# Kernel tuning notes

Measured on AMD Instinct MI355X. Metric: run time of the kernel, lower is better.

## Reference

```python
import jax, jax.numpy as jnp
import numpy as np

NUM_GROUPS = 4   # temporal frames == deformable groups
K = 3            # deformable / fusion kernel size
PAD = 1
MAX_DISP = 7
STRIDE2 = 2


def _conv2d(x, w):
    # 3x3, stride 1, pad 1, no bias, NCHW/OIHW
    return jax.lax.conv_general_dilated(
        x, w, window_strides=(1, 1), padding=((PAD, PAD), (PAD, PAD)),
        dimension_numbers=("NCHW", "OIHW", "NCHW"))


def _correlation(x1, x2):
    """FlowNet/PWC correlation: kernel_size=1, max_displacement=7, stride1=1, stride2=2.
    Output: [B, 49, H, W], mean over channels of shifted dot products."""
    B, C, H, W = x1.shape
    r = MAX_DISP // STRIDE2          # 3 -> 7x7 displacement grid
    m = r * STRIDE2                  # 6 = max shift magnitude
    x2p = jnp.pad(x2, ((0, 0), (0, 0), (m, m), (m, m)))
    outs = []
    for di in range(-r, r + 1):
        for dj in range(-r, r + 1):
            dy, dx = di * STRIDE2, dj * STRIDE2
            sh = x2p[:, :, m + dy:m + dy + H, m + dx:m + dx + W]
            outs.append(jnp.mean(x1 * sh, axis=1))
    return jnp.stack(outs, axis=1)   # [B, 49, H, W]


def _deform_conv(x, offset, weight):
    """Deformable conv v1 (ConvOffset2d): 3x3, stride 1, pad 1, NUM_GROUPS deformable groups.
    offset: [B, G*2*K*K, H, W] laid out as (g, k, {dy,dx})."""
    B, C, H, W = x.shape
    G, K2 = NUM_GROUPS, K * K
    Cg = C // G
    off = offset.reshape(B, G, K2, 2, H, W)
    rel = (jnp.arange(K) - PAD).astype(x.dtype)
    rel_y = jnp.repeat(rel, K).reshape(1, 1, K2, 1, 1)   # kh-major, matches weight flatten
    rel_x = jnp.tile(rel, K).reshape(1, 1, K2, 1, 1)
    iy = jnp.arange(H, dtype=x.dtype).reshape(1, 1, 1, H, 1)
    ix = jnp.arange(W, dtype=x.dtype).reshape(1, 1, 1, 1, W)
    py = iy + rel_y + off[:, :, :, 0]   # [B,G,K2,H,W] sample rows
    px = ix + rel_x + off[:, :, :, 1]   # sample cols
    xg = x.reshape(B, G, Cg, H, W).transpose(0, 1, 3, 4, 2)  # [B,G,H,W,Cg]
    y0 = jnp.floor(py); x0 = jnp.floor(px)
    fy = py - y0; fx = px - x0
    y0 = y0.astype(jnp.int32); x0 = x0.astype(jnp.int32)
    bi = jnp.arange(B).reshape(B, 1, 1, 1, 1)
    gi = jnp.arange(G).reshape(1, G, 1, 1, 1)
    acc = jnp.zeros((B, G, K2, H, W, Cg), x.dtype)
    for dy in (0, 1):
        for dx in (0, 1):
            yy = y0 + dy; xx = x0 + dx
            wgt = (fy if dy else 1.0 - fy) * (fx if dx else 1.0 - fx)
            valid = ((yy >= 0) & (yy < H) & (xx >= 0) & (xx < W)).astype(x.dtype)
            v = xg[bi, gi, jnp.clip(yy, 0, H - 1), jnp.clip(xx, 0, W - 1)]
            acc = acc + v * (wgt * valid)[..., None]
    wr = weight.reshape(weight.shape[0], G, Cg, K2)  # [O,G,Cg,K2]
    return jnp.einsum('bgkhwc,ogck->bohw', acc, wr)


def setup_inputs() -> dict:
    key = jax.random.key(0)
    k0, k1, k2, k3 = jax.random.split(key, 4)
    B, C, H, W = 4, 256, 64, 64
    G = NUM_GROUPS
    inputs = jax.random.normal(k0, (B * G, C, H, W), jnp.float32)
    w_offset = jax.random.normal(k1, (G * 2 * K * K, C + MAX_DISP ** 2, K, K), jnp.float32) * 0.02
    w_def = jax.random.normal(k2, (C, C, K, K), jnp.float32) * 0.02
    w_fusion = jax.random.normal(k3, (C, C * G, K, K), jnp.float32) * 0.02
    return {"inputs": inputs, "w_offset": w_offset, "w_def": w_def,
            "w_fusion": w_fusion, "d1": 0, "d2": 0}


def reference(inputs, w_offset, w_def, w_fusion, d1, d2):
    # d1, d2 are unused by the original forward.
    G = NUM_GROUPS
    y = inputs[G - 1::G]
    _y = jax.lax.stop_gradient(y)
    feats = []
    for ii in range(G - 1):           # n_iter = 1
        x = inputs[ii::G]
        _x = jax.lax.stop_gradient(x)
        corr = _correlation(_x, _y)                       # [B,49,H,W]
        off = _conv2d(jnp.concatenate([x, corr], axis=1), w_offset)
        x = _deform_conv(x, off, w_def)
        feats.append(x)
    return _conv2d(jnp.concatenate(feats + [y], axis=1), w_fusion)
```

## Files before the change

### kernel.cpp

```cpp
#include <hip/hip_runtime.h>

#define HH 64
#define WW 64
#define HW 4096
#define CC 256
#define BB 4
#define GG 4
#define NPAIR 3

typedef __attribute__((ext_vector_type(8))) short short8;
typedef __attribute__((ext_vector_type(4))) float f32x4;
typedef unsigned short ushort_t;

__device__ inline ushort_t f2bf(float x) {
    unsigned int u = __float_as_uint(x);
    unsigned int r = (u + 0x7fffu + ((u >> 16) & 1u)) >> 16;
    return (ushort_t)r;
}
__device__ inline float bflo(unsigned u) { return __uint_as_float(u << 16); }
__device__ inline float bfhi(unsigned u) { return __uint_as_float(u & 0xffff0000u); }

__global__ void prep_all(const float* __restrict__ wd, const float* __restrict__ wo,
                         const float* __restrict__ wf, ushort_t* __restrict__ wdefMF,
                         ushort_t* __restrict__ woffMF, ushort_t* __restrict__ wfusMF) {
    int idx = blockIdx.x * 256 + threadIdx.x;
    if (idx < 589824) {
        int k = idx >> 16;
        int rem = idx & 65535;
        int o = rem >> 8;
        int c = rem & 255;
        wdefMF[idx] = f2bf(wd[((size_t)(o * 256 + c)) * 9 + k]);
        return;
    }
    idx -= 589824;
    if (idx < 230400) {
        int k = idx / (80 * 320);
        int rem = idx % (80 * 320);
        int o = rem / 320;
        int ci = rem % 320;
        woffMF[idx] = (o < 72 && ci < 305) ? f2bf(wo[((size_t)o * 305 + ci) * 9 + k])
                                           : (ushort_t)0;
        return;
    }
    idx -= 230400;
    if (idx < 2359296) {
        int k = idx / (256 * 1024);
        int rem = idx % (256 * 1024);
        int o = rem / 1024;
        int ci = rem % 1024;
        wfusMF[idx] = f2bf(wf[((size_t)o * 1024 + ci) * 9 + k]);
    }
}

__global__ void __launch_bounds__(256) xt_build(const float* __restrict__ in,
                                                ushort_t* __restrict__ XT) {
    __shared__ ushort_t tileT[64][72];
    int hw0 = blockIdx.x * 64;
    int ct = blockIdx.y;
    int z = blockIdx.z;
    int pair = z >> 2, b = z & 3;
    int t = threadIdx.x;
    int cil = t >> 2, q = t & 3;
    const float* sp = in + ((size_t)(b * 4 + pair) * 256 + ct * 64 + cil) * HW + hw0 + q * 16;
#pragma unroll
    for (int i = 0; i < 16; ++i) tileT[q * 16 + i][cil] = f2bf(sp[i]);
    __syncthreads();
    int hwl = t >> 2;
    const uint4* tp = reinterpret_cast<const uint4*>(&tileT[hwl][q * 16]);
    uint4* op = reinterpret_cast<uint4*>(
        &XT[((size_t)z * HW + hw0 + hwl) * 320 + ct * 64 + q * 16]);
    op[0] = tp[0];
    op[1] = tp[1];
}

__global__ void __launch_bounds__(256, 8) corr_partial(const float* __restrict__ in,
                                                       float* __restrict__ P) {
    __shared__ float x1l[8][64];
    __shared__ float x2l[8][7][76];
    int h = blockIdx.x, z = blockIdx.y, cg = blockIdx.z;
    int pair = z >> 2, b = z & 3;
    const float* x1 = in + (size_t)(b * GG + pair) * CC * HW + h * WW;
    const float* x2 = in + (size_t)(b * GG + 3) * CC * HW;
    int tid = threadIdx.x;
    int w = tid & 63;
    int dg = tid >> 6;

    float acc[2][7];
#pragma unroll
    for (int i = 0; i < 2; ++i)
#pragma unroll
        for (int j = 0; j < 7; ++j) acc[i][j] = 0.f;

    for (int c0 = cg * 64; c0 < cg * 64 + 64; c0 += 8) {
        __syncthreads();
#pragma unroll
        for (int idx = tid; idx < 512; idx += 256) {
            int cc = idx >> 6, ww = idx & 63;
            x1l[cc][ww] = x1[(size_t)(c0 + cc) * HW + ww];
        }
        for (int idx = tid; idx < 8 * 7 * 76; idx += 256) {
            int cc = idx / 532;
            int rem = idx - cc * 532;
            int r = rem / 76;
            int cl = rem - r * 76;
            int row = h + 2 * (r - 3);
            int col = cl - 6;
            float v = 0.f;
            if (row >= 0 && row < HH && col >= 0 && col < WW)
                v = x2[(size_t)(c0 + cc) * HW + row * WW + col];
            x2l[cc][r][cl] = v;
        }
        __syncthreads();
#pragma unroll
        for (int cc = 0; cc < 8; ++cc) {
            float x1v = x1l[cc][w];
#pragma unroll
            for (int i = 0; i < 2; ++i) {
                int di = dg * 2 + i;
                if (di < 7) {
#pragma unroll
                    for (int dj = 0; dj < 7; ++dj)
                        acc[i][dj] += x1v * x2l[cc][di][w + 2 * dj];
                }
            }
        }
    }
    float* pp = P + ((size_t)(cg * 12 + z) * 49) * HW + h * WW + w;
#pragma unroll
    for (int i = 0; i < 2; ++i) {
        int di = dg * 2 + i;
        if (di < 7) {
#pragma unroll
            for (int dj = 0; dj < 7; ++dj)
                pp[(size_t)(di * 7 + dj) * HW] = acc[i][dj];
        }
    }
}

__global__ void __launch_bounds__(256) corr_reduce(const float* __restrict__ P,
                                                   ushort_t* __restrict__ XT) {
    int h = blockIdx.x, z = blockIdx.y;
    int tid = threadIdx.x;
    int w = tid & 63;
    int dg = tid >> 6;
    const size_t cgs = (size_t)12 * 49 * HW;
    ushort_t* xrow = XT + ((size_t)z * HW + h * WW + w) * 320;
#pragma unroll
    for (int i = 0; i < 2; ++i) {
        int di = dg * 2 + i;
        if (di < 7) {
#pragma unroll
            for (int dj = 0; dj < 7; ++dj) {
                int d = di * 7 + dj;
                const float* pp = P + ((size_t)z * 49 + d) * HW + h * WW + w;
                float s = pp[0] + pp[cgs] + pp[2 * cgs] + pp[3 * cgs];
                xrow[256 + d] = f2bf(s * (1.f / 256.f));
            }
        }
    }
    if (dg == 3) {
#pragma unroll
        for (int p = 0; p < 15; ++p) xrow[305 + p] = 0;
    }
}

__global__ void __launch_bounds__(256, 2) offconv_mfma(const ushort_t* __restrict__ XT,
                                                       const ushort_t* __restrict__ wmf,
                                                       float* __restrict__ off) {
    __shared__ ushort_t a_lds[9][80][40];
    __shared__ ushort_t b_hal[264][40];
    int lin = (blockIdx.x & 7) * 48 + (blockIdx.x >> 3);
    int z = lin >> 5;
    int n0t = lin & 31;
    int h0 = n0t * 2;
    int t = threadIdx.x;
    int wid = t >> 6;
    int lane = t & 63;
    int l15 = lane & 15;
    int kq = lane >> 4;
    const ushort_t* xtb = XT + (size_t)z * HW * 320;

    f32x4 acc[5][2];
#pragma unroll
    for (int m = 0; m < 5; ++m)
#pragma unroll
        for (int n = 0; n < 2; ++n) acc[m][n] = (f32x4){0.f, 0.f, 0.f, 0.f};

#pragma unroll 1
    for (int cs = 0; cs < 10; ++cs) {
        int ci0 = cs * 32;
        __syncthreads();
        for (int idx = t; idx < 264; idx += 256) {
            int r = idx / 66, c = idx - r * 66;
            int hP = h0 + r - 1, wP = c - 1;
            uint4* dst = reinterpret_cast<uint4*>(&b_hal[idx][0]);
            if (hP >= 0 && hP < HH && wP >= 0 && wP < WW) {
                const uint4* src = reinterpret_cast<const uint4*>(
                    xtb + (size_t)(hP * WW + wP) * 320 + ci0);
                dst[0] = src[0];
                dst[1] = src[1];
                dst[2] = src[2];
                dst[3] = src[3];
            } else {
                uint4 zz = make_uint4(0, 0, 0, 0);
                dst[0] = zz;
                dst[1] = zz;
                dst[2] = zz;
                dst[3] = zz;
            }
        }
        for (int idx = t; idx < 2880; idx += 256) {
            int tp = idx / 320;
            int rem = idx - tp * 320;
            int o = rem >> 2, q = rem & 3;
            *reinterpret_cast<uint4*>(&a_lds[tp][o][q * 8]) =
                *reinterpret_cast<const uint4*>(
                    wmf + ((size_t)tp * 80 + o) * 320 + ci0 + q * 8);
        }
        __syncthreads();
#pragma unroll 1
        for (int tap = 0; tap < 9; ++tap) {
            int kh = tap / 3, kw = tap - kh * 3;
            short8 af[5], bf[2];
#pragma unroll
            for (int m = 0; m < 5; ++m)
                af[m] = *reinterpret_cast<const short8*>(&a_lds[tap][m * 16 + l15][kq * 8]);
#pragma unroll
            for (int n = 0; n < 2; ++n) {
                int p = wid * 32 + n * 16 + l15;
                int pos = ((p >> 6) + kh) * 66 + (p & 63) + kw;
                bf[n] = *reinterpret_cast<const short8*>(&b_hal[pos][kq * 8]);
            }
#pragma unroll
            for (int m = 0; m < 5; ++m)
#pragma unroll
                for (int n = 0; n < 2; ++n)
                    acc[m][n] = __builtin_amdgcn_mfma_f32_16x16x32_bf16(af[m], bf[n],
                                                                        acc[m][n], 0, 0, 0);
        }
    }
    float* ob = off + (size_t)z * 72 * HW + h0 * 64 + wid * 32;
#pragma unroll
    for (int m = 0; m < 5; ++m)
#pragma unroll
        for (int n = 0; n < 2; ++n)
#pragma unroll
            for (int e = 0; e < 4; ++e) {
                int o_l = m * 16 + kq * 4 + e;
                if (o_l < 72) ob[(size_t)o_l * HW + n * 16 + l15] = acc[m][n][e];
            }
}

__global__ void __launch_bounds__(256, 3) deform_mfma(const ushort_t* __restrict__ XT,
                                                      const float* __restrict__ off,
                                                      const ushort_t* __restrict__ wmf,
                                                      ushort_t* __restrict__ FT) {
    __shared__ ushort_t b_lds[64][264];
    int u = blockIdx.x & 7, v = blockIdx.x >> 3;
    int lin = u * 96 + v;
    int z = lin >> 6, h = lin & 63;
    int b = z & 3, pair = z >> 2;

    const ushort_t* xtz = XT + (size_t)z * HW * 320;
    const float* offp = off + (size_t)z * 72 * HW;
    int tid = threadIdx.x;
    int lane = tid & 63;
    int g = tid >> 6;
    int l15 = tid & 15;
    int kq = (tid >> 4) & 3;

    f32x4 acc[4][4];
#pragma unroll
    for (int m = 0; m < 4; ++m)
#pragma unroll
        for (int n = 0; n < 4; ++n) acc[m][n] = (f32x4){0.f, 0.f, 0.f, 0.f};

    for (int k = 0; k < 9; ++k) {
        __syncthreads();
        {
            float oy = offp[(size_t)(g * 18 + k * 2 + 0) * HW + h * WW + lane];
            float ox = offp[(size_t)(g * 18 + k * 2 + 1) * HW + h * WW + lane];
            float py = (float)h + (float)(k / 3 - 1) + oy;
            float px = (float)lane + (float)(k % 3 - 1) + ox;
            float y0f = floorf(py), x0f = floorf(px);
            float fy = py - y0f, fx = px - x0f;
            int y0 = (int)y0f, x0 = (int)x0f;
            int y1 = y0 + 1, x1 = x0 + 1;
            bool vy0 = (y0 >= 0) && (y0 < HH);
            bool vy1 = (y1 >= 0) && (y1 < HH);
            bool vx0 = (x0 >= 0) && (x0 < WW);
            bool vx1 = (x1 >= 0) && (x1 < WW);
            float w00 = (1.f - fy) * (1.f - fx) * ((vy0 && vx0) ? 1.f : 0.f);
            float w01 = (1.f - fy) * fx * ((vy0 && vx1) ? 1.f : 0.f);
            float w10 = fy * (1.f - fx) * ((vy1 && vx0) ? 1.f : 0.f);
            float w11 = fy * fx * ((vy1 && vx1) ? 1.f : 0.f);
            int cy0 = min(max(y0, 0), HH - 1), cy1 = min(max(y1, 0), HH - 1);
            int cx0 = min(max(x0, 0), WW - 1), cx1 = min(max(x1, 0), WW - 1);
            const ushort_t* p00 = xtz + (size_t)(cy0 * WW + cx0) * 320 + g * 64;
            const ushort_t* p01 = xtz + (size_t)(cy0 * WW + cx1) * 320 + g * 64;
            const ushort_t* p10 = xtz + (size_t)(cy1 * WW + cx0) * 320 + g * 64;
            const ushort_t* p11 = xtz + (size_t)(cy1 * WW + cx1) * 320 + g * 64;
#pragma unroll
            for (int c0 = 0; c0 < 64; c0 += 8) {
                uint4 a00 = *reinterpret_cast<const uint4*>(p00 + c0);
                uint4 a01 = *reinterpret_cast<const uint4*>(p01 + c0);
                uint4 a10 = *reinterpret_cast<const uint4*>(p10 + c0);
                uint4 a11 = *reinterpret_cast<const uint4*>(p11 + c0);
                unsigned pw[4];
                const unsigned* u00 = &a00.x;
                const unsigned* u01 = &a01.x;
                const unsigned* u10 = &a10.x;
                const unsigned* u11 = &a11.x;
#pragma unroll
                for (int q = 0; q < 4; ++q) {
                    float s0 = w00 * bflo(u00[q]) + w01 * bflo(u01[q]) +
                               w10 * bflo(u10[q]) + w11 * bflo(u11[q]);
                    float s1 = w00 * bfhi(u00[q]) + w01 * bfhi(u01[q]) +
                               w10 * bfhi(u10[q]) + w11 * bfhi(u11[q]);
                    pw[q] = (unsigned)f2bf(s0) | ((unsigned)f2bf(s1) << 16);
                }
                *reinterpret_cast<uint4*>(&b_lds[lane][g * 64 + c0]) =
                    make_uint4(pw[0], pw[1], pw[2], pw[3]);
            }
        }
        __syncthreads();
        const ushort_t* wkbase = wmf + (size_t)k * 65536 + (size_t)(g * 64) * 256;
#pragma unroll 1
        for (int cs = 0; cs < 8; ++cs) {
            int c0 = cs * 32;
            short8 bfr[4], afr[4];
#pragma unroll
            for (int n = 0; n < 4; ++n)
                bfr[n] = *reinterpret_cast<const short8*>(&b_lds[n * 16 + l15][c0 + kq * 8]);
#pragma unroll
            for (int m = 0; m < 4; ++m)
                afr[m] = *reinterpret_cast<const short8*>(
                    wkbase + (size_t)(m * 16 + l15) * 256 + c0 + kq * 8);
#pragma unroll
            for (int m = 0; m < 4; ++m)
#pragma unroll
                for (int n = 0; n < 4; ++n)
                    acc[m][n] = __builtin_amdgcn_mfma_f32_16x16x32_bf16(afr[m], bfr[n],
                                                                        acc[m][n], 0, 0, 0);
        }
    }
    __syncthreads();
#pragma unroll
    for (int m = 0; m < 4; ++m)
#pragma unroll
        for (int n = 0; n < 4; ++n) {
            unsigned lo = (unsigned)f2bf(acc[m][n][0]) | ((unsigned)f2bf(acc[m][n][1]) << 16);
            unsigned hi = (unsigned)f2bf(acc[m][n][2]) | ((unsigned)f2bf(acc[m][n][3]) << 16);
            uint2 vv = make_uint2(lo, hi);
            *reinterpret_cast<uint2*>(&b_lds[n * 16 + l15][g * 64 + m * 16 + kq * 4]) = vv;
        }
    __syncthreads();
    int wout = tid >> 2, ch = tid & 3;
    ushort_t* dst = FT + ((size_t)b * HW + h * 64 + wout) * 1024 + pair * 256 + ch * 64;
    const ushort_t* srcl = &b_lds[wout][ch * 64];
#pragma unroll
    for (int i = 0; i < 8; ++i) {
        uint4 vv = *reinterpret_cast<const uint4*>(srcl + i * 8);
        *reinterpret_cast<uint4*>(dst + i * 8) = vv;
    }
}

__global__ void __launch_bounds__(256) ft_build_y(const float* __restrict__ in,
                                                  ushort_t* __restrict__ FT) {
    __shared__ ushort_t tileT[64][72];
    int hw0 = blockIdx.x * 64;
    int ct = blockIdx.y;
    int b = blockIdx.z;
    int t = threadIdx.x;
    int cil = t >> 2, q = t & 3;
    const float* sp = in + ((size_t)(b * 4 + 3) * 256 + ct * 64 + cil) * HW + hw0 + q * 16;
#pragma unroll
    for (int i = 0; i < 16; ++i) tileT[q * 16 + i][cil] = f2bf(sp[i]);
    __syncthreads();
    int hwl = t >> 2;
    const uint4* tp = reinterpret_cast<const uint4*>(&tileT[hwl][q * 16]);
    uint4* op = reinterpret_cast<uint4*>(
        &FT[((size_t)b * HW + hw0 + hwl) * 1024 + 768 + ct * 64 + q * 16]);
    op[0] = tp[0];
    op[1] = tp[1];
}

__global__ void __launch_bounds__(256, 2) fusion_mfma(const ushort_t* __restrict__ FT,
                                                      const ushort_t* __restrict__ wmf,
                                                      float* __restrict__ out) {
    __shared__ ushort_t a_lds[9][64][40];
    __shared__ ushort_t b_hal[264][40];
    int lin = ((blockIdx.x & 7) << 6) | (blockIdx.x >> 3);
    int ot = lin & 3;
    int g2 = lin >> 2;
    int n0t = g2 & 31;
    int b = g2 >> 5;
    int o0 = ot * 64;
    int h0 = n0t * 2;
    int t = threadIdx.x;
    int wid = t >> 6;
    int lane = t & 63;
    int l15 = lane & 15;
    int kq = lane >> 4;
    const ushort_t* ftb = FT + (size_t)b * HW * 1024;

    f32x4 acc[4][2];
#pragma unroll
    for (int fm = 0; fm < 4; ++fm)
#pragma unroll
        for (int fn = 0; fn < 2; ++fn) acc[fm][fn] = (f32x4){0.f, 0.f, 0.f, 0.f};

#pragma unroll 1
    for (int cs = 0; cs < 32; ++cs) {
        int ci0 = cs * 32;
        __syncthreads();
        for (int idx = t; idx < 264; idx += 256) {
            int r = idx / 66, c = idx - r * 66;
            int hP = h0 + r - 1, wP = c - 1;
            uint4* dst = reinterpret_cast<uint4*>(&b_hal[idx][0]);
            if (hP >= 0 && hP < HH && wP >= 0 && wP < WW) {
                const uint4* src = reinterpret_cast<const uint4*>(
                    ftb + (size_t)(hP * WW + wP) * 1024 + ci0);
                dst[0] = src[0];
                dst[1] = src[1];
                dst[2] = src[2];
                dst[3] = src[3];
            } else {
                uint4 zz = make_uint4(0, 0, 0, 0);
                dst[0] = zz;
                dst[1] = zz;
                dst[2] = zz;
                dst[3] = zz;
            }
        }
        for (int idx = t; idx < 2304; idx += 256) {
            int tp = idx >> 8;
            int rem = idx & 255;
            int o = rem >> 2, q = rem & 3;
            *reinterpret_cast<uint4*>(&a_lds[tp][o][q * 8]) =
                *reinterpret_cast<const uint4*>(
                    wmf + ((size_t)(tp * 256 + o0 + o) << 10) + ci0 + q * 8);
        }
        __syncthreads();
#pragma unroll 1
        for (int tap = 0; tap < 9; ++tap) {
            int kh = tap / 3, kw = tap - kh * 3;
            short8 af[4], bf[2];
#pragma unroll
            for (int m = 0; m < 4; ++m)
                af[m] = *reinterpret_cast<const short8*>(&a_lds[tap][m * 16 + l15][kq * 8]);
#pragma unroll
            for (int n = 0; n < 2; ++n) {
                int p = wid * 32 + n * 16 + l15;
                int pos = ((p >> 6) + kh) * 66 + (p & 63) + kw;
                bf[n] = *reinterpret_cast<const short8*>(&b_hal[pos][kq * 8]);
            }
#pragma unroll
            for (int m = 0; m < 4; ++m)
#pragma unroll
                for (int n = 0; n < 2; ++n)
                    acc[m][n] = __builtin_amdgcn_mfma_f32_16x16x32_bf16(af[m], bf[n],
                                                                        acc[m][n], 0, 0, 0);
        }
    }
    float* ob = out + ((size_t)b * 256 + o0) * HW + h0 * 64 + wid * 32;
#pragma unroll
    for (int fm = 0; fm < 4; ++fm)
#pragma unroll
        for (int fn = 0; fn < 2; ++fn)
#pragma unroll
            for (int e = 0; e < 4; ++e) {
                int o_l = fm * 16 + 4 * kq + e;
                ob[(size_t)o_l * HW + fn * 16 + l15] = acc[fm][fn][e];
            }
}

extern "C" void kernel_launch(void* const* d_in, const int* in_sizes, int n_in,
                              void* d_out, int out_size, void* d_ws, size_t ws_size,
                              hipStream_t stream) {
    const float* in   = (const float*)d_in[0];
    const float* wOff = (const float*)d_in[1];
    const float* wDef = (const float*)d_in[2];
    const float* wFus = (const float*)d_in[3];
    float* out = (float*)d_out;
    char* base = (char*)d_ws;

    ushort_t* XT     = (ushort_t*)base;
    ushort_t* FT     = (ushort_t*)(base + 31457280);
    float* corrP     = (float*)(base + 31457280);
    float* offB      = (float*)(base + 65011712);
    ushort_t* wdefMF = (ushort_t*)(base + 79167488);
    ushort_t* woffMF = (ushort_t*)(base + 80347136);
    ushort_t* wfusMF = (ushort_t*)(base + 80807936);

    hipLaunchKernelGGL(prep_all, dim3((3179520 + 255) / 256), dim3(256), 0, stream,
                       wDef, wOff, wFus, wdefMF, woffMF, wfusMF);
    hipLaunchKernelGGL(xt_build, dim3(64, 4, 12), dim3(256), 0, stream, in, XT);
    hipLaunchKernelGGL(corr_partial, dim3(64, 12, 4), dim3(256), 0, stream, in, corrP);
    hipLaunchKernelGGL(corr_reduce, dim3(64, 12), dim3(256), 0, stream, corrP, XT);
    hipLaunchKernelGGL(offconv_mfma, dim3(384), dim3(256), 0, stream, XT, woffMF, offB);
    hipLaunchKernelGGL(ft_build_y, dim3(64, 4, 4), dim3(256), 0, stream, in, FT);
    hipLaunchKernelGGL(deform_mfma, dim3(768), dim3(256), 0, stream, XT, offB, wdefMF, FT);
    hipLaunchKernelGGL(fusion_mfma, dim3(512), dim3(256), 0, stream, FT, wfusMF, out);
}
```

Before: 576.7 us.

## Compute correlation as per-row bf16 MFMA matmuls and drop partial-reduce pass

Replaces the scalar fp32 correlation (partial sums over channel groups plus a separate reduce kernel) with one kernel. For each output row and vertical displacement it multiplies the 64x256 bf16 row of x1 by the 64x256 bf16 shifted row of y using MFMA, then keeps only the diagonal band that matches the horizontal shifts. This removes the fp32 partial buffer round trip and one launch, and moves ft_build_y earlier so the bf16 y copy can be reused as the second operand. In exchange it computes unused off-band tile entries, and correlation inputs are now rounded to bf16 rather than kept in fp32.

```diff
diff --git a/kernel.cpp b/kernel.cpp
--- a/kernel.cpp
+++ b/kernel.cpp
@@ -73,94 +73,91 @@
     op[1] = tp[1];
 }
 
-__global__ void __launch_bounds__(256, 8) corr_partial(const float* __restrict__ in,
-                                                       float* __restrict__ P) {
-    __shared__ float x1l[8][64];
-    __shared__ float x2l[8][7][76];
-    int h = blockIdx.x, z = blockIdx.y, cg = blockIdx.z;
-    int pair = z >> 2, b = z & 3;
-    const float* x1 = in + (size_t)(b * GG + pair) * CC * HW + h * WW;
-    const float* x2 = in + (size_t)(b * GG + 3) * CC * HW;
-    int tid = threadIdx.x;
-    int w = tid & 63;
-    int dg = tid >> 6;
-
-    float acc[2][7];
-#pragma unroll
-    for (int i = 0; i < 2; ++i)
-#pragma unroll
-        for (int j = 0; j < 7; ++j) acc[i][j] = 0.f;
-
-    for (int c0 = cg * 64; c0 < cg * 64 + 64; c0 += 8) {
-        __syncthreads();
-#pragma unroll
-        for (int idx = tid; idx < 512; idx += 256) {
-            int cc = idx >> 6, ww = idx & 63;
-            x1l[cc][ww] = x1[(size_t)(c0 + cc) * HW + ww];
-        }
-        for (int idx = tid; idx < 8 * 7 * 76; idx += 256) {
-            int cc = idx / 532;
-            int rem = idx - cc * 532;
-            int r = rem / 76;
-            int cl = rem - r * 76;
-            int row = h + 2 * (r - 3);
-            int col = cl - 6;
-            float v = 0.f;
-            if (row >= 0 && row < HH && col >= 0 && col < WW)
-                v = x2[(size_t)(c0 + cc) * HW + row * WW + col];
-            x2l[cc][r][cl] = v;
-        }
-        __syncthreads();
-#pragma unroll
-        for (int cc = 0; cc < 8; ++cc) {
-            float x1v = x1l[cc][w];
-#pragma unroll
-            for (int i = 0; i < 2; ++i) {
-                int di = dg * 2 + i;
-                if (di < 7) {
-#pragma unroll
-                    for (int dj = 0; dj < 7; ++dj)
-                        acc[i][dj] += x1v * x2l[cc][di][w + 2 * dj];
+__global__ void __launch_bounds__(256) ft_build_y(const float* __restrict__ in,
+                                                  ushort_t* __restrict__ FT) {
+    __shared__ ushort_t tileT[64][72];
+    int hw0 = blockIdx.x * 64;
+    int ct = blockIdx.y;
+    int b = blockIdx.z;
+    int t = threadIdx.x;
+    int cil = t >> 2, q = t & 3;
+    const float* sp = in + ((size_t)(b * 4 + 3) * 256 + ct * 64 + cil) * HW + hw0 + q * 16;
+#pragma unroll
+    for (int i = 0; i < 16; ++i) tileT[q * 16 + i][cil] = f2bf(sp[i]);
+    __syncthreads();
+    int hwl = t >> 2;
+    const uint4* tp = reinterpret_cast<const uint4*>(&tileT[hwl][q * 16]);
+    uint4* op = reinterpret_cast<uint4*>(
+        &FT[((size_t)b * HW + hw0 + hwl) * 1024 + 768 + ct * 64 + q * 16]);
+    op[0] = tp[0];
+    op[1] = tp[1];
+}
+
+__global__ void __launch_bounds__(256, 2) corr_mfma(ushort_t* __restrict__ XT,
+                                                    const ushort_t* __restrict__ FT) {
+    __shared__ ushort_t Al[64][264];
+    __shared__ ushort_t Bl[64][264];
+    int lin = (blockIdx.x & 7) * 96 + (blockIdx.x >> 3);
+    int z = lin >> 6, h = lin & 63;
+    int b = z & 3;
+    int t = threadIdx.x;
+    int ti = t >> 6;
+    int l15 = t & 15, kq = (t >> 4) & 3;
+    const ushort_t* x1 = XT + ((size_t)z * HW + h * 64) * 320;
+    const ushort_t* yb = FT + (size_t)b * HW * 1024 + 768;
+
+    {
+        int p = t >> 2, q = t & 3;
+        ushort_t* xr = XT + ((size_t)z * HW + h * 64 + p) * 320 + 256 + q * 16;
+        uint4 zz = make_uint4(0, 0, 0, 0);
+        *reinterpret_cast<uint4*>(xr) = zz;
+        *reinterpret_cast<uint4*>(xr + 8) = zz;
+    }
+    for (int idx = t; idx < 2048; idx += 256) {
+        int r = idx >> 5, q = idx & 31;
+        *reinterpret_cast<uint4*>(&Al[r][q * 8]) =
+            *reinterpret_cast<const uint4*>(x1 + (size_t)r * 320 + q * 8);
+    }
+    __syncthreads();
+
+    int tj0 = max(ti - 1, 0), tj1 = min(ti + 1, 3);
+#pragma unroll 1
+    for (int di = 0; di < 7; ++di) {
+        int row2 = h + 2 * (di - 3);
+        bool vrow = (row2 >= 0) && (row2 < HH);
+        if (vrow) {
+            for (int idx = t; idx < 2048; idx += 256) {
+                int r = idx >> 5, q = idx & 31;
+                *reinterpret_cast<uint4*>(&Bl[r][q * 8]) =
+                    *reinterpret_cast<const uint4*>(
+                        yb + ((size_t)(row2 * 64 + r)) * 1024 + q * 8);
+            }
+        }
+        __syncthreads();
+        if (vrow) {
+#pragma unroll 1
+            for (int tj = tj0; tj <= tj1; ++tj) {
+                f32x4 acc = (f32x4){0.f, 0.f, 0.f, 0.f};
+#pragma unroll
+                for (int cs = 0; cs < 8; ++cs) {
+                    int c0 = cs * 32;
+                    short8 a = *reinterpret_cast<const short8*>(&Al[ti * 16 + l15][c0 + kq * 8]);
+                    short8 bb = *reinterpret_cast<const short8*>(&Bl[tj * 16 + l15][c0 + kq * 8]);
+                    acc = __builtin_amdgcn_mfma_f32_16x16x32_bf16(a, bb, acc, 0, 0, 0);
                 }
-            }
-        }
-    }
-    float* pp = P + ((size_t)(cg * 12 + z) * 49) * HW + h * WW + w;
-#pragma unroll
-    for (int i = 0; i < 2; ++i) {
-        int di = dg * 2 + i;
-        if (di < 7) {
-#pragma unroll
-            for (int dj = 0; dj < 7; ++dj)
-                pp[(size_t)(di * 7 + dj) * HW] = acc[i][dj];
-        }
-    }
-}
-
-__global__ void __launch_bounds__(256) corr_reduce(const float* __restrict__ P,
-                                                   ushort_t* __restrict__ XT) {
-    int h = blockIdx.x, z = blockIdx.y;
-    int tid = threadIdx.x;
-    int w = tid & 63;
-    int dg = tid >> 6;
-    const size_t cgs = (size_t)12 * 49 * HW;
-    ushort_t* xrow = XT + ((size_t)z * HW + h * WW + w) * 320;
-#pragma unroll
-    for (int i = 0; i < 2; ++i) {
-        int di = dg * 2 + i;
-        if (di < 7) {
-#pragma unroll
-            for (int dj = 0; dj < 7; ++dj) {
-                int d = di * 7 + dj;
-                const float* pp = P + ((size_t)z * 49 + d) * HW + h * WW + w;
-                float s = pp[0] + pp[cgs] + pp[2 * cgs] + pp[3 * cgs];
-                xrow[256 + d] = f2bf(s * (1.f / 256.f));
-            }
-        }
-    }
-    if (dg == 3) {
-#pragma unroll
-        for (int p = 0; p < 15; ++p) xrow[305 + p] = 0;
+#pragma unroll
+                for (int e = 0; e < 4; ++e) {
+                    int row = ti * 16 + 4 * kq + e;
+                    int col = tj * 16 + l15;
+                    int d = col - row + 6;
+                    if (d >= 0 && d <= 12 && !(d & 1)) {
+                        XT[((size_t)z * HW + h * 64 + row) * 320 + 256 + di * 7 + (d >> 1)] =
+                            f2bf(acc[e] * (1.f / 256.f));
+                    }
+                }
+            }
+        }
+        __syncthreads();
     }
 }
 
@@ -365,26 +362,6 @@
     }
 }
 
-__global__ void __launch_bounds__(256) ft_build_y(const float* __restrict__ in,
-                                                  ushort_t* __restrict__ FT) {
-    __shared__ ushort_t tileT[64][72];
-    int hw0 = blockIdx.x * 64;
-    int ct = blockIdx.y;
-    int b = blockIdx.z;
-    int t = threadIdx.x;
-    int cil = t >> 2, q = t & 3;
-    const float* sp = in + ((size_t)(b * 4 + 3) * 256 + ct * 64 + cil) * HW + hw0 + q * 16;
-#pragma unroll
-    for (int i = 0; i < 16; ++i) tileT[q * 16 + i][cil] = f2bf(sp[i]);
-    __syncthreads();
-    int hwl = t >> 2;
-    const uint4* tp = reinterpret_cast<const uint4*>(&tileT[hwl][q * 16]);
-    uint4* op = reinterpret_cast<uint4*>(
-        &FT[((size_t)b * HW + hw0 + hwl) * 1024 + 768 + ct * 64 + q * 16]);
-    op[0] = tp[0];
-    op[1] = tp[1];
-}
-
 __global__ void __launch_bounds__(256, 2) fusion_mfma(const ushort_t* __restrict__ FT,
                                                       const ushort_t* __restrict__ wmf,
                                                       float* __restrict__ out) {
@@ -487,7 +464,6 @@
 
     ushort_t* XT     = (ushort_t*)base;
     ushort_t* FT     = (ushort_t*)(base + 31457280);
-    float* corrP     = (float*)(base + 31457280);
     float* offB      = (float*)(base + 65011712);
     ushort_t* wdefMF = (ushort_t*)(base + 79167488);
     ushort_t* woffMF = (ushort_t*)(base + 80347136);
@@ -496,10 +472,9 @@
     hipLaunchKernelGGL(prep_all, dim3((3179520 + 255) / 256), dim3(256), 0, stream,
                        wDef, wOff, wFus, wdefMF, woffMF, wfusMF);
     hipLaunchKernelGGL(xt_build, dim3(64, 4, 12), dim3(256), 0, stream, in, XT);
-    hipLaunchKernelGGL(corr_partial, dim3(64, 12, 4), dim3(256), 0, stream, in, corrP);
-    hipLaunchKernelGGL(corr_reduce, dim3(64, 12), dim3(256), 0, stream, corrP, XT);
+    hipLaunchKernelGGL(ft_build_y, dim3(64, 4, 4), dim3(256), 0, stream, in, FT);
+    hipLaunchKernelGGL(corr_mfma, dim3(768), dim3(256), 0, stream, XT, FT);
     hipLaunchKernelGGL(offconv_mfma, dim3(384), dim3(256), 0, stream, XT, woffMF, offB);
-    hipLaunchKernelGGL(ft_build_y, dim3(64, 4, 4), dim3(256), 0, stream, in, FT);
     hipLaunchKernelGGL(deform_mfma, dim3(768), dim3(256), 0, stream, XT, offB, wdefMF, FT);
     hipLaunchKernelGGL(fusion_mfma, dim3(512), dim3(256), 0, stream, FT, wfusMF, out);
 }
```

New measurement: 473.9 us. 1.22x faster.
